# Kernel optimization log

Measured on AMD Instinct MI355X. Metric: run time of the kernel, lower is better.

Reference implementation:

```python
import jax, jax.numpy as jnp
import numpy as np

N, R, A = 50000, 1000, 5000          # node_size, rel_size, attr_size
D, H = 256, 4                        # input_dim == output_dim, n_heads
DH = D // H                          # per-head dim (64)
RD, AD = 64, 64                      # rel_dim, attr_dim
L = 2                                # num_layers
E, ER, EA = 200000, 150000, 150000   # ent-ent, ent-rel, ent-attr edges


def _seg_softmax(v, seg, n):
    # softmax over entries sharing the same segment (= tf.sparse.softmax per row)
    m = jax.ops.segment_max(v, seg, num_segments=n)
    e = jnp.exp(v - m[seg])
    s = jax.ops.segment_sum(e, seg, num_segments=n)
    return e / s[seg]


def _concept(emb, idx, n):
    # rel/attr adjacency with all-ones values -> row softmax == mean over neighbors,
    # then relu (matches tf.sparse.softmax + sparse_dense_matmul + relu)
    row, col = idx[:, 0], idx[:, 1]
    w = _seg_softmax(jnp.ones(idx.shape[0], emb.dtype), row, n)
    return jax.nn.relu(jax.ops.segment_sum(w[:, None] * emb[col], row, num_segments=n))


def setup_inputs() -> dict:
    key = jax.random.key(0)
    ks = jax.random.split(key, 12)
    ent_emb = jax.random.normal(ks[0], (N, D), jnp.float32) * 0.1
    rel_emb = jax.random.normal(ks[1], (R, RD), jnp.float32) * 0.1
    attr_emb = jax.random.normal(ks[2], (A, AD), jnp.float32) * 0.1
    ent_kernels = jax.random.normal(ks[3], (L, H, DH, DH), jnp.float32) * 0.08
    ent_attn_kernels = jax.random.normal(ks[4], (L, H, 2 * DH), jnp.float32) * 0.08
    edge_index = jax.random.randint(ks[5], (E, 2), 0, N, dtype=jnp.int32)
    edge_val = jax.random.uniform(ks[6], (E,), jnp.float32)
    rel_index = jnp.stack([jax.random.randint(ks[7], (ER,), 0, N, dtype=jnp.int32),
                           jax.random.randint(ks[8], (ER,), 0, R, dtype=jnp.int32)], axis=1)
    attr_index = jnp.stack([jax.random.randint(ks[9], (EA,), 0, N, dtype=jnp.int32),
                            jax.random.randint(ks[10], (EA,), 0, A, dtype=jnp.int32)], axis=1)
    return {"ent_emb": ent_emb, "rel_emb": rel_emb, "attr_emb": attr_emb,
            "ent_kernels": ent_kernels, "ent_attn_kernels": ent_attn_kernels,
            "edge_val": edge_val, "edge_index": edge_index,
            "rel_index": rel_index, "attr_index": attr_index}


def reference(ent_emb, rel_emb, attr_emb, ent_kernels, ent_attn_kernels,
              edge_val, edge_index, rel_index, attr_index):
    concept_rel = _concept(rel_emb, rel_index, N)    # (N, RD)
    concept_attr = _concept(attr_emb, attr_index, N) # (N, AD)

    row, col = edge_index[:, 0], edge_index[:, 1]
    # pre-aggregation: row-softmaxed weighted adjacency @ ent_emb
    w = _seg_softmax(edge_val, row, N)
    h = jax.ops.segment_sum(w[:, None] * ent_emb[col], row, num_segments=N)  # (N, D)

    outs = []
    for l in range(L):
        h = jax.nn.relu(h)
        hh = h.reshape(N, H, DH)           # per-head features
        nb = hh[col]                       # (E, H, DH) neighbor gather
        sf = hh[row]                       # (E, H, DH) self gather
        Wk = ent_kernels[l]                # (H, DH, DH)
        wn = jax.nn.relu(jnp.einsum('ehd,hdf->ehf', nb, Wk))
        ws = jax.nn.relu(jnp.einsum('ehd,hdf->ehf', sf, Wk))
        ak = ent_attn_kernels[l]           # (H, 2*DH)
        attn = (jnp.einsum('ehd,hd->eh', ws, ak[:, :DH])
                + jnp.einsum('ehd,hd->eh', wn, ak[:, DH:]))
        attn = jax.nn.leaky_relu(attn, negative_slope=0.3)
        attn = jax.nn.softmax(attn, axis=0)       # tf.nn.softmax over all E edges (per head)
        attn = _seg_softmax(attn, row, N)         # tf.sparse.softmax per row
        # note: aggregation uses the UN-transformed neighbor features (as in source)
        h = jnp.tanh(jax.ops.segment_sum(nb * attn[:, :, None], row,
                                         num_segments=N).reshape(N, D))
        outs.append(h)

    grat_out = jnp.concatenate(outs, axis=-1)                       # (N, L*D)
    ent_out = jnp.concatenate([grat_out, concept_rel, concept_attr], axis=-1)
    conc = jnp.concatenate([concept_rel, concept_attr], axis=-1)
    return ent_out, conc
```

## Files before the change

### kernel.cpp

```cpp
#include <hip/hip_runtime.h>
#include <hip/hip_bf16.h>

#define N_  50000
#define R_  1000
#define A_  5000
#define D_  256
#define H_  4
#define DH_ 64
#define E_  200000
#define ER_ 150000
#define EA_ 150000

__device__ __forceinline__ unsigned f2key(float f) {
    unsigned b = __float_as_uint(f);
    return (b & 0x80000000u) ? ~b : (b | 0x80000000u);
}
__device__ __forceinline__ float key2f(unsigned k) {
    unsigned b = (k & 0x80000000u) ? (k ^ 0x80000000u) : ~k;
    return __uint_as_float(b);
}

__global__ void k_concept_accum(const int* __restrict__ idx, const float* __restrict__ emb,
                                float* __restrict__ sum, int* __restrict__ deg, int nE) {
    int gid = blockIdx.x * blockDim.x + threadIdx.x;
    if (gid >= nE * 64) return;
    int e = gid >> 6, d = gid & 63;
    int row = idx[2 * e], col = idx[2 * e + 1];
    atomicAdd(&sum[row * 64 + d], emb[col * 64 + d]);
    if (d == 0) atomicAdd(&deg[row], 1);
}

__global__ void k_concept_final(const float* __restrict__ sum_rel, const int* __restrict__ deg_rel,
                                const float* __restrict__ sum_attr, const int* __restrict__ deg_attr,
                                float* __restrict__ out) {
    int gid = blockIdx.x * blockDim.x + threadIdx.x;
    if (gid >= N_ * 128) return;
    int n = gid >> 7, d = gid & 127;
    float v;
    if (d < 64) {
        int dg = deg_rel[n];
        v = dg > 0 ? sum_rel[n * 64 + d] / (float)dg : 0.f;
    } else {
        int dg = deg_attr[n];
        v = dg > 0 ? sum_attr[n * 64 + (d - 64)] / (float)dg : 0.f;
    }
    v = fmaxf(v, 0.f);
    out[(size_t)n * 640 + 512 + d] = v;
    out[(size_t)N_ * 640 + (size_t)n * 128 + d] = v;
}

__global__ void k_h0_denom(const int* __restrict__ eidx, const float* __restrict__ eval,
                           float* __restrict__ z0) {
    int e = blockIdx.x * blockDim.x + threadIdx.x;
    if (e >= E_) return;
    atomicAdd(&z0[eidx[2 * e]], expf(eval[e]));
}

__global__ void k_h0_scatter(const int* __restrict__ eidx, const float* __restrict__ eval,
                             const float* __restrict__ z0, const float* __restrict__ ent_emb,
                             float* __restrict__ h0) {
    long long gid = (long long)blockIdx.x * blockDim.x + threadIdx.x;
    if (gid >= (long long)E_ * 256) return;
    int e = (int)(gid >> 8), d = (int)(gid & 255);
    int row = eidx[2 * e], col = eidx[2 * e + 1];
    float w = expf(eval[e]) / z0[row];
    atomicAdd(&h0[(size_t)row * 256 + d], w * ent_emb[(size_t)col * 256 + d]);
}

__global__ void k_transform(const float* __restrict__ h, const float* __restrict__ Wk,
                            const float* __restrict__ ak, float* __restrict__ s1,
                            float* __restrict__ s2) {
    int n = blockIdx.x;
    int lane = threadIdx.x & 63;
    int head = threadIdx.x >> 6;
    const float* W = Wk + head * 64 * 64;
    const float* hr = h + (size_t)n * 256 + head * 64;
    float t = 0.f;
    for (int d = 0; d < 64; ++d) {
        float hv = fmaxf(hr[d], 0.f);
        t += hv * W[d * 64 + lane];
    }
    t = fmaxf(t, 0.f);
    float p1 = t * ak[head * 128 + lane];
    float p2 = t * ak[head * 128 + 64 + lane];
    for (int s = 32; s >= 1; s >>= 1) {
        p1 += __shfl_xor(p1, s, 64);
        p2 += __shfl_xor(p2, s, 64);
    }
    if (lane == 0) { s1[n * 4 + head] = p1; s2[n * 4 + head] = p2; }
}

__global__ void k_attn1(const int* __restrict__ eidx,
                        const float* __restrict__ s1, const float* __restrict__ s2,
                        float* __restrict__ a_arr, unsigned* __restrict__ Mkey) {
    __shared__ unsigned smax[4];
    int tid = threadIdx.x;
    if (tid < 4) smax[tid] = 0u;
    __syncthreads();
    long long gid = (long long)blockIdx.x * blockDim.x + tid;
    if (gid < (long long)E_ * 4) {
        int e = (int)(gid >> 2), hh = (int)(gid & 3);
        float a = s1[eidx[2 * e] * 4 + hh] + s2[eidx[2 * e + 1] * 4 + hh];
        a = (a > 0.f) ? a : 0.3f * a;
        a_arr[gid] = a;
        atomicMax(&smax[hh], f2key(a));
    }
    __syncthreads();
    if (tid < 4 && smax[tid]) atomicMax(&Mkey[tid], smax[tid]);
}

__global__ void k_attn2(float* __restrict__ a_arr, const unsigned* __restrict__ Mkey,
                        float* __restrict__ S) {
    __shared__ float ssum[4];
    int tid = threadIdx.x;
    if (tid < 4) ssum[tid] = 0.f;
    __syncthreads();
    long long gid = (long long)blockIdx.x * blockDim.x + tid;
    if (gid < (long long)E_ * 4) {
        int hh = (int)(gid & 3);
        float v = expf(a_arr[gid] - key2f(Mkey[hh]));
        a_arr[gid] = v;
        atomicAdd(&ssum[hh], v);
    }
    __syncthreads();
    if (tid < 4 && ssum[tid] != 0.f) atomicAdd(&S[tid], ssum[tid]);
}

__global__ void k_attn3(const int* __restrict__ eidx, float* __restrict__ a_arr,
                        const float* __restrict__ S, float* __restrict__ zl) {
    long long gid = (long long)blockIdx.x * blockDim.x + threadIdx.x;
    if (gid >= (long long)E_ * 4) return;
    int e = (int)(gid >> 2), hh = (int)(gid & 3);
    float v = a_arr[gid] / S[hh];
    float ev = expf(v);
    a_arr[gid] = ev;
    atomicAdd(&zl[eidx[2 * e] * 4 + hh], ev);
}

__global__ void k_aggr_scatter(const int* __restrict__ eidx, const float* __restrict__ a_arr,
                               const float* __restrict__ zl, const float* __restrict__ h_in,
                               float* __restrict__ acc) {
    long long gid = (long long)blockIdx.x * blockDim.x + threadIdx.x;
    if (gid >= (long long)E_ * 256) return;
    int e = (int)(gid >> 8), d = (int)(gid & 255);
    int head = d >> 6;
    int row = eidx[2 * e], col = eidx[2 * e + 1];
    float w = a_arr[e * 4 + head] / zl[row * 4 + head];
    float hv = fmaxf(h_in[(size_t)col * 256 + d], 0.f);
    atomicAdd(&acc[(size_t)row * 256 + d], w * hv);
}

__global__ void k_finalize(float* __restrict__ acc, float* __restrict__ out, int layer) {
    int gid = blockIdx.x * blockDim.x + threadIdx.x;
    if (gid >= N_ * 256) return;
    int n = gid >> 8, d = gid & 255;
    float o = tanhf(acc[gid]);
    acc[gid] = o;
    out[(size_t)n * 640 + layer * 256 + d] = o;
}

static inline size_t align256(size_t x) { return (x + 255) & ~(size_t)255; }

extern "C" void kernel_launch(void* const* d_in, const int* in_sizes, int n_in,
                              void* d_out, int out_size, void* d_ws, size_t ws_size,
                              hipStream_t stream) {
    const float* ent_emb     = (const float*)d_in[0];
    const float* rel_emb     = (const float*)d_in[1];
    const float* attr_emb    = (const float*)d_in[2];
    const float* ent_kernels = (const float*)d_in[3];
    const float* ent_attn    = (const float*)d_in[4];
    const float* edge_val    = (const float*)d_in[5];
    const int*   edge_index  = (const int*)d_in[6];
    const int*   rel_index   = (const int*)d_in[7];
    const int*   attr_index  = (const int*)d_in[8];
    float* out = (float*)d_out;

    char* w = (char*)d_ws;
    size_t off = 0;
    auto carve = [&](size_t bytes) { void* p = w + off; off += align256(bytes); return p; };

    size_t gA_beg = off;
    float* sum_rel  = (float*)carve((size_t)N_ * 64 * 4);
    float* sum_attr = (float*)carve((size_t)N_ * 64 * 4);
    int*   deg_rel  = (int*)carve((size_t)N_ * 4);
    int*   deg_attr = (int*)carve((size_t)N_ * 4);
    float* z0       = (float*)carve((size_t)N_ * 4);
    size_t gA_size = off - gA_beg;

    float* s1    = (float*)carve((size_t)N_ * 4 * 4);
    float* s2    = (float*)carve((size_t)N_ * 4 * 4);
    float* a_arr = (float*)carve((size_t)E_ * 4 * 4);

    size_t gB_beg = off;
    float*    zl   = (float*)carve((size_t)N_ * 4 * 4);
    unsigned* Mkey = (unsigned*)carve(4 * 4);
    float*    S    = (float*)carve(4 * 4);
    size_t gB_size = off - gB_beg;

    float* h_a = (float*)carve((size_t)N_ * 256 * 4);
    float* h_b = (float*)carve((size_t)N_ * 256 * 4);

    hipMemsetAsync(w + gA_beg, 0, gA_size, stream);
    k_concept_accum<<<(ER_ * 64 + 255) / 256, 256, 0, stream>>>(rel_index, rel_emb, sum_rel, deg_rel, ER_);
    k_concept_accum<<<(EA_ * 64 + 255) / 256, 256, 0, stream>>>(attr_index, attr_emb, sum_attr, deg_attr, EA_);
    k_concept_final<<<(N_ * 128 + 255) / 256, 256, 0, stream>>>(sum_rel, deg_rel, sum_attr, deg_attr, out);

    k_h0_denom<<<(E_ + 255) / 256, 256, 0, stream>>>(edge_index, edge_val, z0);
    hipMemsetAsync(h_a, 0, (size_t)N_ * 256 * 4, stream);
    {
        long long tot = (long long)E_ * 256;
        k_h0_scatter<<<(unsigned)((tot + 255) / 256), 256, 0, stream>>>(edge_index, edge_val, z0, ent_emb, h_a);
    }

    for (int l = 0; l < 2; ++l) {
        float* h_in = (l == 0) ? h_a : h_b;
        float* acc  = (l == 0) ? h_b : h_a;
        k_transform<<<N_, 256, 0, stream>>>(h_in, ent_kernels + (size_t)l * H_ * 64 * 64,
                                            ent_attn + (size_t)l * H_ * 128, s1, s2);
        hipMemsetAsync(w + gB_beg, 0, gB_size, stream);
        hipMemsetAsync(acc, 0, (size_t)N_ * 256 * 4, stream);
        k_attn1<<<(E_ * 4 + 255) / 256, 256, 0, stream>>>(edge_index, s1, s2, a_arr, Mkey);
        k_attn2<<<(E_ * 4 + 255) / 256, 256, 0, stream>>>(a_arr, Mkey, S);
        k_attn3<<<(E_ * 4 + 255) / 256, 256, 0, stream>>>(edge_index, a_arr, S, zl);
        {
            long long tot = (long long)E_ * 256;
            k_aggr_scatter<<<(unsigned)((tot + 255) / 256), 256, 0, stream>>>(edge_index, a_arr, zl, h_in, acc);
        }
        k_finalize<<<(N_ * 256 + 255) / 256, 256, 0, stream>>>(acc, out, l);
    }
}
```

Baseline: 1.291 ms.

## Vectorize scatter kernels with float4 and tile node transform with register weights

Each thread in the scatter and elementwise kernels now handles four contiguous floats, loaded as float4, which cuts per-edge index and weight loads by four. The transform kernel now processes 32 nodes per block. It keeps the per-head weight column in registers and stages relu'd node features in shared memory, so the weight matrix is no longer reloaded once per node. Index arithmetic is narrowed to 32-bit. Holding 64 floats per thread in registers may lower occupancy.

```diff
diff --git a/kernel.cpp b/kernel.cpp
--- a/kernel.cpp
+++ b/kernel.cpp
@@ -10,6 +10,7 @@
 #define E_  200000
 #define ER_ 150000
 #define EA_ 150000
+#define TNB 32
 
 __device__ __forceinline__ unsigned f2key(float f) {
     unsigned b = __float_as_uint(f);
@@ -23,30 +24,42 @@
 __global__ void k_concept_accum(const int* __restrict__ idx, const float* __restrict__ emb,
                                 float* __restrict__ sum, int* __restrict__ deg, int nE) {
     int gid = blockIdx.x * blockDim.x + threadIdx.x;
-    if (gid >= nE * 64) return;
-    int e = gid >> 6, d = gid & 63;
+    if (gid >= nE * 16) return;
+    int e = gid >> 4, q = gid & 15;
     int row = idx[2 * e], col = idx[2 * e + 1];
-    atomicAdd(&sum[row * 64 + d], emb[col * 64 + d]);
-    if (d == 0) atomicAdd(&deg[row], 1);
+    float4 v = *(const float4*)(emb + (size_t)col * 64 + q * 4);
+    float* dst = sum + (size_t)row * 64 + q * 4;
+    atomicAdd(dst + 0, v.x);
+    atomicAdd(dst + 1, v.y);
+    atomicAdd(dst + 2, v.z);
+    atomicAdd(dst + 3, v.w);
+    if (q == 0) atomicAdd(&deg[row], 1);
 }
 
 __global__ void k_concept_final(const float* __restrict__ sum_rel, const int* __restrict__ deg_rel,
                                 const float* __restrict__ sum_attr, const int* __restrict__ deg_attr,
                                 float* __restrict__ out) {
     int gid = blockIdx.x * blockDim.x + threadIdx.x;
-    if (gid >= N_ * 128) return;
-    int n = gid >> 7, d = gid & 127;
-    float v;
-    if (d < 64) {
+    if (gid >= N_ * 32) return;
+    int n = gid >> 5, q = gid & 31;
+    int d0 = q * 4;
+    float4 v;
+    float inv;
+    if (d0 < 64) {
         int dg = deg_rel[n];
-        v = dg > 0 ? sum_rel[n * 64 + d] / (float)dg : 0.f;
+        inv = dg > 0 ? 1.f / (float)dg : 0.f;
+        v = *(const float4*)(sum_rel + (size_t)n * 64 + d0);
     } else {
         int dg = deg_attr[n];
-        v = dg > 0 ? sum_attr[n * 64 + (d - 64)] / (float)dg : 0.f;
-    }
-    v = fmaxf(v, 0.f);
-    out[(size_t)n * 640 + 512 + d] = v;
-    out[(size_t)N_ * 640 + (size_t)n * 128 + d] = v;
+        inv = dg > 0 ? 1.f / (float)dg : 0.f;
+        v = *(const float4*)(sum_attr + (size_t)n * 64 + (d0 - 64));
+    }
+    v.x = fmaxf(v.x * inv, 0.f);
+    v.y = fmaxf(v.y * inv, 0.f);
+    v.z = fmaxf(v.z * inv, 0.f);
+    v.w = fmaxf(v.w * inv, 0.f);
+    *(float4*)(out + (size_t)n * 640 + 512 + d0) = v;
+    *(float4*)(out + (size_t)N_ * 640 + (size_t)n * 128 + d0) = v;
 }
 
 __global__ void k_h0_denom(const int* __restrict__ eidx, const float* __restrict__ eval,
@@ -59,35 +72,76 @@
 __global__ void k_h0_scatter(const int* __restrict__ eidx, const float* __restrict__ eval,
                              const float* __restrict__ z0, const float* __restrict__ ent_emb,
                              float* __restrict__ h0) {
-    long long gid = (long long)blockIdx.x * blockDim.x + threadIdx.x;
-    if (gid >= (long long)E_ * 256) return;
-    int e = (int)(gid >> 8), d = (int)(gid & 255);
+    int gid = blockIdx.x * blockDim.x + threadIdx.x;
+    if (gid >= E_ * 64) return;
+    int e = gid >> 6, q = gid & 63;
     int row = eidx[2 * e], col = eidx[2 * e + 1];
     float w = expf(eval[e]) / z0[row];
-    atomicAdd(&h0[(size_t)row * 256 + d], w * ent_emb[(size_t)col * 256 + d]);
-}
-
-__global__ void k_transform(const float* __restrict__ h, const float* __restrict__ Wk,
-                            const float* __restrict__ ak, float* __restrict__ s1,
-                            float* __restrict__ s2) {
-    int n = blockIdx.x;
-    int lane = threadIdx.x & 63;
-    int head = threadIdx.x >> 6;
-    const float* W = Wk + head * 64 * 64;
-    const float* hr = h + (size_t)n * 256 + head * 64;
-    float t = 0.f;
-    for (int d = 0; d < 64; ++d) {
-        float hv = fmaxf(hr[d], 0.f);
-        t += hv * W[d * 64 + lane];
-    }
-    t = fmaxf(t, 0.f);
-    float p1 = t * ak[head * 128 + lane];
-    float p2 = t * ak[head * 128 + 64 + lane];
-    for (int s = 32; s >= 1; s >>= 1) {
-        p1 += __shfl_xor(p1, s, 64);
-        p2 += __shfl_xor(p2, s, 64);
-    }
-    if (lane == 0) { s1[n * 4 + head] = p1; s2[n * 4 + head] = p2; }
+    float4 v = *(const float4*)(ent_emb + (size_t)col * 256 + q * 4);
+    float* dst = h0 + (size_t)row * 256 + q * 4;
+    atomicAdd(dst + 0, w * v.x);
+    atomicAdd(dst + 1, w * v.y);
+    atomicAdd(dst + 2, w * v.z);
+    atomicAdd(dst + 3, w * v.w);
+}
+
+__global__ void __launch_bounds__(256) k_transform(
+        const float* __restrict__ h, const float* __restrict__ Wk,
+        const float* __restrict__ ak, float* __restrict__ s1, float* __restrict__ s2) {
+    __shared__ float hs[TNB * 256];
+    int tid = threadIdx.x;
+    int lane = tid & 63;
+    int head = tid >> 6;
+    int nbase = blockIdx.x * TNB;
+    int nnodes = min(TNB, N_ - nbase);
+
+    float Wreg[64];
+    const float* W = Wk + head * 4096;
+    #pragma unroll
+    for (int d = 0; d < 64; ++d) Wreg[d] = W[d * 64 + lane];
+
+    const float4* src = (const float4*)(h + (size_t)nbase * 256);
+    for (int i = tid; i < nnodes * 64; i += 256) {
+        float4 v = src[i];
+        v.x = fmaxf(v.x, 0.f);
+        v.y = fmaxf(v.y, 0.f);
+        v.z = fmaxf(v.z, 0.f);
+        v.w = fmaxf(v.w, 0.f);
+        ((float4*)hs)[i] = v;
+    }
+    __syncthreads();
+
+    const float* akh = ak + head * 128;
+    float a1 = akh[lane], a2 = akh[64 + lane];
+
+    for (int n = 0; n < nnodes; ++n) {
+        const float* hr = hs + n * 256 + head * 64;
+        float t0 = 0.f, t1 = 0.f;
+        #pragma unroll
+        for (int d = 0; d < 64; d += 8) {
+            float4 u = *(const float4*)(hr + d);
+            float4 v = *(const float4*)(hr + d + 4);
+            t0 = fmaf(u.x, Wreg[d + 0], t0);
+            t1 = fmaf(u.y, Wreg[d + 1], t1);
+            t0 = fmaf(u.z, Wreg[d + 2], t0);
+            t1 = fmaf(u.w, Wreg[d + 3], t1);
+            t0 = fmaf(v.x, Wreg[d + 4], t0);
+            t1 = fmaf(v.y, Wreg[d + 5], t1);
+            t0 = fmaf(v.z, Wreg[d + 6], t0);
+            t1 = fmaf(v.w, Wreg[d + 7], t1);
+        }
+        float t = fmaxf(t0 + t1, 0.f);
+        float p1 = t * a1, p2 = t * a2;
+        #pragma unroll
+        for (int s = 32; s >= 1; s >>= 1) {
+            p1 += __shfl_xor(p1, s, 64);
+            p2 += __shfl_xor(p2, s, 64);
+        }
+        if (lane == 0) {
+            s1[(nbase + n) * 4 + head] = p1;
+            s2[(nbase + n) * 4 + head] = p2;
+        }
+    }
 }
 
 __global__ void k_attn1(const int* __restrict__ eidx,
@@ -97,9 +151,9 @@
     int tid = threadIdx.x;
     if (tid < 4) smax[tid] = 0u;
     __syncthreads();
-    long long gid = (long long)blockIdx.x * blockDim.x + tid;
-    if (gid < (long long)E_ * 4) {
-        int e = (int)(gid >> 2), hh = (int)(gid & 3);
+    int gid = blockIdx.x * blockDim.x + tid;
+    if (gid < E_ * 4) {
+        int e = gid >> 2, hh = gid & 3;
         float a = s1[eidx[2 * e] * 4 + hh] + s2[eidx[2 * e + 1] * 4 + hh];
         a = (a > 0.f) ? a : 0.3f * a;
         a_arr[gid] = a;
@@ -115,9 +169,9 @@
     int tid = threadIdx.x;
     if (tid < 4) ssum[tid] = 0.f;
     __syncthreads();
-    long long gid = (long long)blockIdx.x * blockDim.x + tid;
-    if (gid < (long long)E_ * 4) {
-        int hh = (int)(gid & 3);
+    int gid = blockIdx.x * blockDim.x + tid;
+    if (gid < E_ * 4) {
+        int hh = gid & 3;
         float v = expf(a_arr[gid] - key2f(Mkey[hh]));
         a_arr[gid] = v;
         atomicAdd(&ssum[hh], v);
@@ -128,9 +182,9 @@
 
 __global__ void k_attn3(const int* __restrict__ eidx, float* __restrict__ a_arr,
                         const float* __restrict__ S, float* __restrict__ zl) {
-    long long gid = (long long)blockIdx.x * blockDim.x + threadIdx.x;
-    if (gid >= (long long)E_ * 4) return;
-    int e = (int)(gid >> 2), hh = (int)(gid & 3);
+    int gid = blockIdx.x * blockDim.x + threadIdx.x;
+    if (gid >= E_ * 4) return;
+    int e = gid >> 2, hh = gid & 3;
     float v = a_arr[gid] / S[hh];
     float ev = expf(v);
     a_arr[gid] = ev;
@@ -140,23 +194,31 @@
 __global__ void k_aggr_scatter(const int* __restrict__ eidx, const float* __restrict__ a_arr,
                                const float* __restrict__ zl, const float* __restrict__ h_in,
                                float* __restrict__ acc) {
-    long long gid = (long long)blockIdx.x * blockDim.x + threadIdx.x;
-    if (gid >= (long long)E_ * 256) return;
-    int e = (int)(gid >> 8), d = (int)(gid & 255);
-    int head = d >> 6;
+    int gid = blockIdx.x * blockDim.x + threadIdx.x;
+    if (gid >= E_ * 64) return;
+    int e = gid >> 6, q = gid & 63;
+    int head = q >> 4;
     int row = eidx[2 * e], col = eidx[2 * e + 1];
     float w = a_arr[e * 4 + head] / zl[row * 4 + head];
-    float hv = fmaxf(h_in[(size_t)col * 256 + d], 0.f);
-    atomicAdd(&acc[(size_t)row * 256 + d], w * hv);
+    float4 v = *(const float4*)(h_in + (size_t)col * 256 + q * 4);
+    float* dst = acc + (size_t)row * 256 + q * 4;
+    atomicAdd(dst + 0, w * fmaxf(v.x, 0.f));
+    atomicAdd(dst + 1, w * fmaxf(v.y, 0.f));
+    atomicAdd(dst + 2, w * fmaxf(v.z, 0.f));
+    atomicAdd(dst + 3, w * fmaxf(v.w, 0.f));
 }
 
 __global__ void k_finalize(float* __restrict__ acc, float* __restrict__ out, int layer) {
     int gid = blockIdx.x * blockDim.x + threadIdx.x;
-    if (gid >= N_ * 256) return;
-    int n = gid >> 8, d = gid & 255;
-    float o = tanhf(acc[gid]);
-    acc[gid] = o;
-    out[(size_t)n * 640 + layer * 256 + d] = o;
+    if (gid >= N_ * 64) return;
+    int n = gid >> 6, q = gid & 63;
+    float4 v = ((const float4*)acc)[gid];
+    v.x = tanhf(v.x);
+    v.y = tanhf(v.y);
+    v.z = tanhf(v.z);
+    v.w = tanhf(v.w);
+    ((float4*)acc)[gid] = v;
+    *(float4*)(out + (size_t)n * 640 + layer * 256 + q * 4) = v;
 }
 
 static inline size_t align256(size_t x) { return (x + 255) & ~(size_t)255; }
@@ -201,31 +263,25 @@
     float* h_b = (float*)carve((size_t)N_ * 256 * 4);
 
     hipMemsetAsync(w + gA_beg, 0, gA_size, stream);
-    k_concept_accum<<<(ER_ * 64 + 255) / 256, 256, 0, stream>>>(rel_index, rel_emb, sum_rel, deg_rel, ER_);
-    k_concept_accum<<<(EA_ * 64 + 255) / 256, 256, 0, stream>>>(attr_index, attr_emb, sum_attr, deg_attr, EA_);
-    k_concept_final<<<(N_ * 128 + 255) / 256, 256, 0, stream>>>(sum_rel, deg_rel, sum_attr, deg_attr, out);
+    k_concept_accum<<<(ER_ * 16 + 255) / 256, 256, 0, stream>>>(rel_index, rel_emb, sum_rel, deg_rel, ER_);
+    k_concept_accum<<<(EA_ * 16 + 255) / 256, 256, 0, stream>>>(attr_index, attr_emb, sum_attr, deg_attr, EA_);
+    k_concept_final<<<(N_ * 32 + 255) / 256, 256, 0, stream>>>(sum_rel, deg_rel, sum_attr, deg_attr, out);
 
     k_h0_denom<<<(E_ + 255) / 256, 256, 0, stream>>>(edge_index, edge_val, z0);
     hipMemsetAsync(h_a, 0, (size_t)N_ * 256 * 4, stream);
-    {
-        long long tot = (long long)E_ * 256;
-        k_h0_scatter<<<(unsigned)((tot + 255) / 256), 256, 0, stream>>>(edge_index, edge_val, z0, ent_emb, h_a);
-    }
+    k_h0_scatter<<<(E_ * 64 + 255) / 256, 256, 0, stream>>>(edge_index, edge_val, z0, ent_emb, h_a);
 
     for (int l = 0; l < 2; ++l) {
         float* h_in = (l == 0) ? h_a : h_b;
         float* acc  = (l == 0) ? h_b : h_a;
-        k_transform<<<N_, 256, 0, stream>>>(h_in, ent_kernels + (size_t)l * H_ * 64 * 64,
-                                            ent_attn + (size_t)l * H_ * 128, s1, s2);
+        k_transform<<<(N_ + TNB - 1) / TNB, 256, 0, stream>>>(
+            h_in, ent_kernels + (size_t)l * H_ * 64 * 64, ent_attn + (size_t)l * H_ * 128, s1, s2);
         hipMemsetAsync(w + gB_beg, 0, gB_size, stream);
         hipMemsetAsync(acc, 0, (size_t)N_ * 256 * 4, stream);
         k_attn1<<<(E_ * 4 + 255) / 256, 256, 0, stream>>>(edge_index, s1, s2, a_arr, Mkey);
         k_attn2<<<(E_ * 4 + 255) / 256, 256, 0, stream>>>(a_arr, Mkey, S);
         k_attn3<<<(E_ * 4 + 255) / 256, 256, 0, stream>>>(edge_index, a_arr, S, zl);
-        {
-            long long tot = (long long)E_ * 256;
-            k_aggr_scatter<<<(unsigned)((tot + 255) / 256), 256, 0, stream>>>(edge_index, a_arr, zl, h_in, acc);
-        }
-        k_finalize<<<(N_ * 256 + 255) / 256, 256, 0, stream>>>(acc, out, l);
-    }
-}
+        k_aggr_scatter<<<(E_ * 64 + 255) / 256, 256, 0, stream>>>(edge_index, a_arr, zl, h_in, acc);
+        k_finalize<<<(N_ * 64 + 255) / 256, 256, 0, stream>>>(acc, out, l);
+    }
+}
```

Result: slower. 2.727 ms (+111.2%).
